# Kernel optimization log

Hardware: AMD Instinct MI355X
Metric: run time of the kernel (lower is better)

Reference implementation:

```python
import jax, jax.numpy as jnp
import numpy as np

EXPERT_NUM = 8
SEQ_LEN = 4096
FREQ_LEN = SEQ_LEN // 2 + 1


def setup_inputs() -> dict:
    key = jax.random.key(0)
    ks = jax.random.split(key, 6)
    B, C = 32, 8
    x = jax.random.normal(ks[0], (B, C, SEQ_LEN), dtype=jnp.float32)
    raw = jax.random.uniform(ks[1], (EXPERT_NUM - 1,), dtype=jnp.float32)
    s1 = 1.0 / np.sqrt(FREQ_LEN)
    W1 = jax.random.uniform(ks[2], (FREQ_LEN, FREQ_LEN), jnp.float32, -s1, s1)
    b1 = jax.random.uniform(ks[3], (FREQ_LEN,), jnp.float32, -s1, s1)
    W2 = jax.random.uniform(ks[4], (EXPERT_NUM, FREQ_LEN), jnp.float32, -s1, s1)
    b2 = jax.random.uniform(ks[5], (EXPERT_NUM,), jnp.float32, -s1, s1)
    return {"x": x, "raw": raw, "W1": W1, "b1": b1, "W2": W2, "b2": b2}


def reference(x, raw, W1, b1, W2, b2):
    # instance norm over seq dim (unbiased variance, like torch.var default)
    x_mean = jnp.mean(x, axis=2, keepdims=True)
    xc = x - x_mean
    n = x.shape[2]
    x_var = jnp.sum(xc * xc, axis=2, keepdims=True) / (n - 1) + 1e-5
    xn = xc / jnp.sqrt(x_var)

    freq_x = jnp.fft.rfft(xn, axis=-1)            # [B, C, F] complex
    F_ = freq_x.shape[-1]

    # sorted sigmoid boundaries -> integer band edges (non-differentiable cast)
    b = jnp.sort(jax.nn.sigmoid(raw))
    boundaries = jnp.concatenate([jnp.zeros(1, x.dtype), b, jnp.ones(1, x.dtype)])
    idx = jnp.floor(jax.lax.stop_gradient(boundaries) * F_).astype(jnp.int32)
    idx = idx.at[-1].set(F_)

    # band-pass masks for all experts at once: [E, F]
    fpos = jnp.arange(F_)
    mask = (fpos[None, :] >= idx[:-1, None]) & (fpos[None, :] < idx[1:, None])

    # per-expert frequency components: [B, E, C, F]
    comp = freq_x[:, None, :, :] * mask[None, :, None, :].astype(freq_x.dtype)
    expert_outputs = jnp.fft.irfft(comp, n=SEQ_LEN, axis=-1)  # [B, E, C, L]

    # gating on channel-averaged magnitude spectrum
    gating_input = jnp.mean(jnp.abs(freq_x), axis=1)          # [B, F]
    h = jax.nn.relu(gating_input @ W1.T + b1)
    gating_scores = jax.nn.softmax(h @ W2.T + b2, axis=-1)    # [B, E]

    # gated combine in frequency domain, then single iFFT
    gate_c = gating_scores.astype(freq_x.dtype)
    combined_freq = jnp.einsum('becf,be->bcf', comp, gate_c)
    combined = jnp.fft.irfft(combined_freq, n=SEQ_LEN, axis=-1)
    combined = combined * jnp.sqrt(x_var) + x_mean
    return combined, boundaries, gating_scores, expert_outputs
```

## Files before the change

kernel.cpp:

```cpp
#include <hip/hip_runtime.h>
#include <hip/hip_bf16.h>


using cplx = float2;
typedef float nfloat2 __attribute__((ext_vector_type(2)));

static constexpr int BB = 32, CCH = 8, LL = 4096, FF = 2049, EE = 8;

static constexpr size_t WS_FREQ  = 0;
static constexpr size_t WS_MEAN  = WS_FREQ + (size_t)BB * CCH * FF * 2;
static constexpr size_t WS_SIGMA = WS_MEAN + 256;
static constexpr size_t WS_H     = WS_SIGMA + 256;
static constexpr size_t WS_IDX   = WS_H + (size_t)BB * FF;
static constexpr size_t WS_EOF   = WS_IDX + 16;

static constexpr size_t OUT_COMB = 0;
static constexpr size_t OUT_BND  = (size_t)BB * CCH * LL;
static constexpr size_t OUT_GATE = OUT_BND + 9;
static constexpr size_t OUT_EXP  = OUT_GATE + (size_t)BB * EE;

__device__ float2 g_W2048[2048];
__device__ float2 g_U[2049];
__device__ int    g_tabcnt = 0;
__device__ float  g_gi[BB * FF];

#define PHI(i) ((i) + ((i) >> 5))
__device__ __forceinline__ int scat(int n) {
  return ((n & 3) << 9) | (((n >> 2) & 7) << 6) | (((n >> 5) & 7) << 3) | (n >> 8);
}

template <bool INV>
__device__ __forceinline__ void dft8(float* zr, float* zi) {
  const float C = 0.70710678118654752f;
  float s0r = zr[0] + zr[4], s0i = zi[0] + zi[4];
  float d0r = zr[0] - zr[4], d0i = zi[0] - zi[4];
  float s1r = zr[2] + zr[6], s1i = zi[2] + zi[6];
  float d1r = zr[2] - zr[6], d1i = zi[2] - zi[6];
  float E0r = s0r + s1r, E0i = s0i + s1i;
  float E2r = s0r - s1r, E2i = s0i - s1i;
  float E1r, E1i, E3r, E3i;
  if (!INV) { E1r = d0r + d1i; E1i = d0i - d1r; E3r = d0r - d1i; E3i = d0i + d1r; }
  else      { E1r = d0r - d1i; E1i = d0i + d1r; E3r = d0r + d1i; E3i = d0i - d1r; }
  float t0r = zr[1] + zr[5], t0i = zi[1] + zi[5];
  float e0r = zr[1] - zr[5], e0i = zi[1] - zi[5];
  float t1r = zr[3] + zr[7], t1i = zi[3] + zi[7];
  float e1r = zr[3] - zr[7], e1i = zi[3] - zi[7];
  float O0r = t0r + t1r, O0i = t0i + t1i;
  float O2r = t0r - t1r, O2i = t0i - t1i;
  float O1r, O1i, O3r, O3i;
  if (!INV) { O1r = e0r + e1i; O1i = e0i - e1r; O3r = e0r - e1i; O3i = e0i + e1r; }
  else      { O1r = e0r - e1i; O1i = e0i + e1r; O3r = e0r + e1i; O3i = e0i - e1r; }
  float w1r, w1i, w2r, w2i, w3r, w3i;
  if (!INV) {
    w1r = C * (O1r + O1i); w1i = C * (O1i - O1r);
    w2r = O2i;             w2i = -O2r;
    w3r = C * (O3i - O3r); w3i = -C * (O3r + O3i);
  } else {
    w1r = C * (O1r - O1i); w1i = C * (O1i + O1r);
    w2r = -O2i;            w2i = O2r;
    w3r = -C * (O3r + O3i); w3i = C * (O3r - O3i);
  }
  zr[0] = E0r + O0r; zi[0] = E0i + O0i;
  zr[4] = E0r - O0r; zi[4] = E0i - O0i;
  zr[1] = E1r + w1r; zi[1] = E1i + w1i;
  zr[5] = E1r - w1r; zi[5] = E1i - w1i;
  zr[2] = E2r + w2r; zi[2] = E2i + w2i;
  zr[6] = E2r - w2r; zi[6] = E2i - w2i;
  zr[3] = E3r + w3r; zi[3] = E3i + w3i;
  zr[7] = E3r - w3r; zi[7] = E3i - w3i;
}

template <bool INV>
__device__ __forceinline__ void dft4(float* zr, float* zi) {
  float s0r = zr[0] + zr[2], s0i = zi[0] + zi[2];
  float d0r = zr[0] - zr[2], d0i = zi[0] - zi[2];
  float s1r = zr[1] + zr[3], s1i = zi[1] + zi[3];
  float d1r = zr[1] - zr[3], d1i = zi[1] - zi[3];
  zr[0] = s0r + s1r; zi[0] = s0i + s1i;
  zr[2] = s0r - s1r; zi[2] = s0i - s1i;
  if (!INV) { zr[1] = d0r + d1i; zi[1] = d0i - d1r; zr[3] = d0r - d1i; zi[3] = d0i + d1r; }
  else      { zr[1] = d0r - d1i; zi[1] = d0i + d1r; zr[3] = d0r + d1i; zi[3] = d0i - d1r; }
}

template <bool INV>
__device__ void fftr8(float* ZR, float* ZI, const cplx* __restrict__ W, int t) {
  float zr[8], zi[8];
  {
    int base = 8 * t;
#pragma unroll
    for (int m = 0; m < 8; ++m) { int i = PHI(base + m); zr[m] = ZR[i]; zi[m] = ZI[i]; }
    dft8<INV>(zr, zi);
#pragma unroll
    for (int m = 0; m < 8; ++m) { int i = PHI(base + m); ZR[i] = zr[m]; ZI[i] = zi[m]; }
  }
  __syncthreads();
  {
    int g = t & 31, p = t >> 5;
    int base = 64 * g + p;
#pragma unroll
    for (int m = 0; m < 8; ++m) { int i = PHI(base + 8 * m); zr[m] = ZR[i]; zi[m] = ZI[i]; }
#pragma unroll
    for (int m = 1; m < 8; ++m) {
      cplx w = W[32 * m * p];
      float wi = INV ? -w.y : w.y;
      float xr = zr[m] * w.x - zi[m] * wi;
      float xi = zr[m] * wi + zi[m] * w.x;
      zr[m] = xr; zi[m] = xi;
    }
    dft8<INV>(zr, zi);
#pragma unroll
    for (int m = 0; m < 8; ++m) { int i = PHI(base + 8 * m); ZR[i] = zr[m]; ZI[i] = zi[m]; }
  }
  __syncthreads();
  {
    int g = t & 3, p = t >> 2;
    int base = 512 * g + p;
#pragma unroll
    for (int m = 0; m < 8; ++m) { int i = PHI(base + 64 * m); zr[m] = ZR[i]; zi[m] = ZI[i]; }
#pragma unroll
    for (int m = 1; m < 8; ++m) {
      cplx w = W[4 * m * p];
      float wi = INV ? -w.y : w.y;
      float xr = zr[m] * w.x - zi[m] * wi;
      float xi = zr[m] * wi + zi[m] * w.x;
      zr[m] = xr; zi[m] = xi;
    }
    dft8<INV>(zr, zi);
#pragma unroll
    for (int m = 0; m < 8; ++m) { int i = PHI(base + 64 * m); ZR[i] = zr[m]; ZI[i] = zi[m]; }
  }
  __syncthreads();
  {
#pragma unroll
    for (int h = 0; h < 2; ++h) {
      int p = t + (h << 8);
      float yr[4], yi[4];
#pragma unroll
      for (int m = 0; m < 4; ++m) { int i = PHI(p + 512 * m); yr[m] = ZR[i]; yi[m] = ZI[i]; }
#pragma unroll
      for (int m = 1; m < 4; ++m) {
        cplx w = W[m * p];
        float wi = INV ? -w.y : w.y;
        float xr = yr[m] * w.x - yi[m] * wi;
        float xi = yr[m] * wi + yi[m] * w.x;
        yr[m] = xr; yi[m] = xi;
      }
      dft4<INV>(yr, yi);
#pragma unroll
      for (int m = 0; m < 4; ++m) { int i = PHI(p + 512 * m); ZR[i] = yr[m]; ZI[i] = yi[m]; }
    }
  }
  __syncthreads();
}

__device__ __forceinline__ void expert_ifft(const float* __restrict__ ws,
                                            float* __restrict__ out,
                                            float* ZR, float* ZI,
                                            int bc, int j, int t) {
  const int b = bc >> 3, c = bc & 7;
  const cplx* freq = (const cplx*)ws + (size_t)bc * FF;
  const int*  idxp = (const int*)(ws + WS_IDX);
  const int lo = idxp[j], hi = idxp[j + 1];

#pragma unroll
  for (int u = 0; u < 8; ++u) {
    int k  = t + (u << 8);
    int km = 2048 - k;
    cplx A = make_float2(0.f, 0.f), Bv = make_float2(0.f, 0.f);
    if (k >= lo && k < hi)   A  = freq[k];
    if (km >= lo && km < hi) Bv = freq[km];
    float Px = A.x - Bv.x, Py = A.y + Bv.y;
    float Qx = A.x + Bv.x, Qy = A.y - Bv.y;
    cplx uk = g_U[k];
    float cs = uk.x, sn = -uk.y;
    float Xox = 0.5f * (cs * Px - sn * Py);
    float Xoy = 0.5f * (cs * Py + sn * Px);
    int i = PHI(scat(k));
    ZR[i] = 0.5f * Qx - Xoy;
    ZI[i] = 0.5f * Qy + Xox;
  }
  __syncthreads();

  fftr8<true>(ZR, ZI, g_W2048, t);

  const float mul = 1.0f / 2048.0f;
  float* op = out + OUT_EXP + (((size_t)(b * EE + j) * CCH + c) * LL);
  if (t == 0) __builtin_nontemporal_store(ZR[PHI(0)] * mul, op);
#pragma unroll
  for (int u = 0; u < 8; ++u) {
    int n = t + (u << 8);
    if (n < 2047) {
      nfloat2 o;
      o.x = ZI[PHI(n)] * mul;
      o.y = ZR[PHI(n + 1)] * mul;
      __builtin_nontemporal_store(o, (nfloat2*)(op + 2 * n + 1));
    } else {
      __builtin_nontemporal_store(ZI[PHI(2047)] * mul, op + 4095);
    }
  }
}

__global__ __launch_bounds__(256) void k_fwd(const float* __restrict__ x,
                                             const float* __restrict__ raw,
                                             float* __restrict__ ws,
                                             float* __restrict__ out) {
  const int p = blockIdx.x, t = threadIdx.x;

  if (p >= 256) {
    if (p < 273) {
      if (__hip_atomic_load(&g_tabcnt, __ATOMIC_RELAXED, __HIP_MEMORY_SCOPE_AGENT) < 17) {
        if (p < 264) {
          int jj = (p - 256) * 256 + t;
          float sn, cs;
          sincosf(-6.283185307179586f * (float)jj / 2048.0f, &sn, &cs);
          g_W2048[jj] = make_float2(cs, sn);
        } else {
          int k = (p - 264) * 256 + t;
          if (k < FF) {
            float sn, cs;
            sincosf(-3.14159265358979323846f * (float)k / 2048.0f, &sn, &cs);
            g_U[k] = make_float2(cs, sn);
          }
        }
        __syncthreads();
        if (t == 0) {
          __threadfence();
          __hip_atomic_fetch_add(&g_tabcnt, 1, __ATOMIC_RELEASE, __HIP_MEMORY_SCOPE_AGENT);
        }
      }
    } else if (p == 273) {
      __shared__ int idx_s[9];
      if (t == 0) {
        float v[7];
        for (int i = 0; i < 7; ++i) v[i] = 1.0f / (1.0f + expf(-raw[i]));
        for (int a = 1; a < 7; ++a) {
          float key = v[a];
          int q = a - 1;
          while (q >= 0 && v[q] > key) { v[q + 1] = v[q]; --q; }
          v[q + 1] = key;
        }
        float bnd[9];
        bnd[0] = 0.0f; bnd[8] = 1.0f;
        for (int i = 0; i < 7; ++i) bnd[i + 1] = v[i];
        int* wi = (int*)(ws + WS_IDX);
        for (int e = 0; e < 9; ++e) {
          int id = (int)floorf(bnd[e] * (float)FF);
          if (e == 8) id = FF;
          idx_s[e] = id;
          wi[e] = id;
          out[OUT_BND + e] = bnd[e];
        }
      }
      __syncthreads();
      int* eof = (int*)(ws + WS_EOF);
      for (int f = t; f < FF; f += 256) {
        int e = 0;
        for (int q = 1; q < 8; ++q)
          if (f >= idx_s[q]) e = q;
        eof[f] = e;
      }
    } else {
      float4* hp = (float4*)(ws + WS_H);
      const float4 z4 = make_float4(0.f, 0.f, 0.f, 0.f);
      for (int i = (p - 274) * 256 + t; i < 16392; i += 8 * 256) hp[i] = z4;
    }
    return;
  }

  __shared__ float ZR[2112], ZI[2112];
  __shared__ float red[8];
  const int bc = p;
  const int b  = bc >> 3;
  const int lane = t & 63, wid = t >> 6;
  const float2* xp2 = (const float2*)(x + (size_t)bc * LL);

  float2 v[8];
  float sum = 0.f;
#pragma unroll
  for (int u = 0; u < 8; ++u) {
    v[u] = xp2[t + (u << 8)];
    sum += v[u].x + v[u].y;
  }
#pragma unroll
  for (int off = 32; off > 0; off >>= 1) sum += __shfl_down(sum, off, 64);
  if (lane == 0) red[wid] = sum;
  __syncthreads();
  const float mean = (red[0] + red[1] + red[2] + red[3]) * (1.0f / 4096.0f);

  float ss = 0.f;
#pragma unroll
  for (int u = 0; u < 8; ++u) {
    float dx = v[u].x - mean, dy = v[u].y - mean;
    ss += dx * dx + dy * dy;
  }
#pragma unroll
  for (int off = 32; off > 0; off >>= 1) ss += __shfl_down(ss, off, 64);
  if (lane == 0) red[4 + wid] = ss;
  __syncthreads();
  const float var   = (red[4] + red[5] + red[6] + red[7]) / 4095.0f + 1e-5f;
  const float sigma = sqrtf(var);
  const float inv   = 1.0f / sigma;
  if (t == 0) {
    ws[WS_MEAN + bc]  = mean;
    ws[WS_SIGMA + bc] = sigma;
  }

#pragma unroll
  for (int u = 0; u < 8; ++u) {
    int n = t + (u << 8);
    int i = PHI(scat(n));
    ZR[i] = (v[u].x - mean) * inv;
    ZI[i] = (v[u].y - mean) * inv;
  }
  if (t == 0) {
    while (__hip_atomic_load(&g_tabcnt, __ATOMIC_ACQUIRE, __HIP_MEMORY_SCOPE_AGENT) < 17) {
      __builtin_amdgcn_s_sleep(8);
    }
  }
  __syncthreads();

  fftr8<false>(ZR, ZI, g_W2048, t);

  cplx* freq = (cplx*)ws + (size_t)bc * FF;
#pragma unroll
  for (int u = 0; u < 9; ++u) {
    int k = t + (u << 8);
    if (k > 2048) break;
    int ka = k & 2047, km = (2048 - k) & 2047;
    float Zkr = ZR[PHI(ka)], Zki = ZI[PHI(ka)];
    float Zmr = ZR[PHI(km)], Zmi = ZI[PHI(km)];
    float fex = 0.5f * (Zkr + Zmr);
    float fey = 0.5f * (Zki - Zmi);
    float fox = 0.5f * (Zki + Zmi);
    float foy = -0.5f * (Zkr - Zmr);
    cplx uk = g_U[k];
    float rx = fex + uk.x * fox - uk.y * foy;
    float ry = fey + uk.x * foy + uk.y * fox;
    freq[k] = make_float2(rx, ry);
    atomicAdd(&g_gi[(size_t)b * FF + k], 0.125f * sqrtf(rx * rx + ry * ry));
  }
}

__global__ __launch_bounds__(256) void k_mid(const float* __restrict__ W1,
                                             float* __restrict__ ws,
                                             float* __restrict__ out) {
  __shared__ float SM[4224];
  const int p = blockIdx.x, t = threadIdx.x;

  if (p < 1089) {
    float* W1s = SM;
    float* gis = SM + 2112;
    const int i0 = (p % 33) * 64;
    const int il = t & 63, bg = t >> 6;
    float acc[8] = {0, 0, 0, 0, 0, 0, 0, 0};
    const int fbeg = (p / 33) * 64;
    const int fend = min(fbeg + 64, FF);
    for (int f0 = fbeg; f0 < fend; f0 += 32) {
      for (int q = t; q < 64 * 32; q += 256) {
        int r = q >> 5, cc = q & 31;
        int gi_i = i0 + r, gf = f0 + cc;
        W1s[r * 33 + cc] = (gi_i < FF && gf < FF) ? W1[(size_t)gi_i * FF + gf] : 0.f;
      }
      for (int q = t; q < 32 * 32; q += 256) {
        int bb = q >> 5, cc = q & 31;
        int gf = f0 + cc;
        gis[bb * 33 + cc] = (gf < FF) ? g_gi[(size_t)bb * FF + gf] : 0.f;
      }
      __syncthreads();
#pragma unroll 8
      for (int cc = 0; cc < 32; ++cc) {
        float wv = W1s[il * 33 + cc];
#pragma unroll
        for (int j = 0; j < 8; ++j) acc[j] += wv * gis[(bg * 8 + j) * 33 + cc];
      }
      __syncthreads();
    }
    int ii = i0 + il;
    if (ii < FF) {
#pragma unroll
      for (int j = 0; j < 8; ++j)
        atomicAdd(&ws[WS_H + (size_t)(bg * 8 + j) * FF + ii], acc[j]);
    }
    return;
  }
  if (p < 1096) return;

  const int e   = p - 1096;
  const int xcd = e & 7, s = e >> 3;
  const int grp = s >> 3, j = s & 7;
  const int bc  = (grp << 3) | xcd;
  expert_ifft(ws, out, SM, SM + 2112, bc, j, t);
}

__global__ __launch_bounds__(256) void k_comb(const float* __restrict__ b1,
                                              const float* __restrict__ W2,
                                              const float* __restrict__ b2,
                                              const float* __restrict__ ws,
                                              float* __restrict__ out) {
  __shared__ float ZR[2112], ZI[2112];
  __shared__ float red[4][8];
  __shared__ float lg[8];
  __shared__ float gates_s[8];
  const int q = blockIdx.x, t = threadIdx.x;
  const int bc = q;
  const int b  = bc >> 3, c = bc & 7;
  const int lane = t & 63, wid = t >> 6;

  {
    int i = q * 256 + t;
    g_gi[i] = 0.f;
    if (i < 32) g_gi[65536 + i] = 0.f;
  }

  float pacc[8] = {0, 0, 0, 0, 0, 0, 0, 0};
  const float* hrow = ws + WS_H + (size_t)b * FF;
  for (int f = t; f < FF; f += 256) {
    float hv = fmaxf(hrow[f] + b1[f], 0.f);
#pragma unroll
    for (int e = 0; e < 8; ++e) pacc[e] += hv * W2[(size_t)e * FF + f];
  }
#pragma unroll
  for (int off = 32; off > 0; off >>= 1) {
#pragma unroll
    for (int e = 0; e < 8; ++e) pacc[e] += __shfl_down(pacc[e], off, 64);
  }
  if (lane == 0) {
#pragma unroll
    for (int e = 0; e < 8; ++e) red[wid][e] = pacc[e];
  }
  __syncthreads();
  if (t < 8) lg[t] = red[0][t] + red[1][t] + red[2][t] + red[3][t] + b2[t];
  __syncthreads();
  if (t < 8) {
    float mx = lg[0];
#pragma unroll
    for (int r2 = 1; r2 < 8; ++r2) mx = fmaxf(mx, lg[r2]);
    float sm = 0.f;
#pragma unroll
    for (int r2 = 0; r2 < 8; ++r2) sm += expf(lg[r2] - mx);
    float g = expf(lg[t] - mx) / sm;
    gates_s[t] = g;
    if (c == 0) out[OUT_GATE + (size_t)b * 8 + t] = g;
  }
  __syncthreads();

  const cplx* freq = (const cplx*)ws + (size_t)bc * FF;
  const int*  eof  = (const int*)(ws + WS_EOF);

#pragma unroll
  for (int u = 0; u < 8; ++u) {
    int k  = t + (u << 8);
    int km = 2048 - k;
    cplx A  = freq[k];
    cplx Bv = freq[km];
    float gk = gates_s[eof[k]], gm = gates_s[eof[km]];
    A.x *= gk; A.y *= gk; Bv.x *= gm; Bv.y *= gm;
    float Px = A.x - Bv.x, Py = A.y + Bv.y;
    float Qx = A.x + Bv.x, Qy = A.y - Bv.y;
    cplx uk = g_U[k];
    float cs = uk.x, sn = -uk.y;
    float Xox = 0.5f * (cs * Px - sn * Py);
    float Xoy = 0.5f * (cs * Py + sn * Px);
    int i = PHI(scat(k));
    ZR[i] = 0.5f * Qx - Xoy;
    ZI[i] = 0.5f * Qy + Xox;
  }
  __syncthreads();

  fftr8<true>(ZR, ZI, g_W2048, t);

  const float mul = ws[WS_SIGMA + bc] * (1.0f / 2048.0f);
  const float add = ws[WS_MEAN + bc];
  nfloat2* op = (nfloat2*)(out + OUT_COMB + (size_t)bc * LL);
#pragma unroll
  for (int u = 0; u < 8; ++u) {
    int n = t + (u << 8);
    nfloat2 o;
    o.x = ZR[PHI(n)] * mul + add;
    o.y = ZI[PHI(n)] * mul + add;
    __builtin_nontemporal_store(o, op + n);
  }
}

extern "C" void kernel_launch(void* const* d_in, const int* in_sizes, int n_in,
                              void* d_out, int out_size, void* d_ws, size_t ws_size,
                              hipStream_t stream) {
  const float* x   = (const float*)d_in[0];
  const float* raw = (const float*)d_in[1];
  const float* W1  = (const float*)d_in[2];
  const float* b1  = (const float*)d_in[3];
  const float* W2  = (const float*)d_in[4];
  const float* b2  = (const float*)d_in[5];
  float* out = (float*)d_out;
  float* ws  = (float*)d_ws;

  k_fwd<<<282, 256, 0, stream>>>(x, raw, ws, out);
  k_mid<<<1096 + 2048, 256, 0, stream>>>(W1, ws, out);
  k_comb<<<256, 256, 0, stream>>>(b1, W2, b2, ws, out);
}
```

Baseline: 130.6 us.

## Fuse ReLU and W2 projection into GEMV blocks, pack two rows per FFT block

The W1 GEMV no longer uses 1089 split-K blocks that atomically accumulate into a zeroed H buffer. It now runs 33 blocks, each covering the full K range for 64 outputs. Each block applies bias and ReLU and computes a partial W2 projection into g_part, which k_comb sums to get the gating logits. This removes the H zeroing, the atomics and the per-row W2 dot products in k_comb. The forward and combine FFT kernels now process two (b,c) rows per 512-thread block, and the expert-iFFT row mapping is adjusted. The risk is that only 33 blocks stream the 16 MB W1 matrix, so GEMV parallelism may be too low to saturate bandwidth.

```diff
diff --git a/kernel.cpp b/kernel.cpp
--- a/kernel.cpp
+++ b/kernel.cpp
@@ -10,8 +10,7 @@
 static constexpr size_t WS_FREQ  = 0;
 static constexpr size_t WS_MEAN  = WS_FREQ + (size_t)BB * CCH * FF * 2;
 static constexpr size_t WS_SIGMA = WS_MEAN + 256;
-static constexpr size_t WS_H     = WS_SIGMA + 256;
-static constexpr size_t WS_IDX   = WS_H + (size_t)BB * FF;
+static constexpr size_t WS_IDX   = WS_SIGMA + 256;
 static constexpr size_t WS_EOF   = WS_IDX + 16;
 
 static constexpr size_t OUT_COMB = 0;
@@ -23,6 +22,7 @@
 __device__ float2 g_U[2049];
 __device__ int    g_tabcnt = 0;
 __device__ float  g_gi[BB * FF];
+__device__ float  g_part[33 * 256];
 
 #define PHI(i) ((i) + ((i) >> 5))
 __device__ __forceinline__ int scat(int n) {
@@ -200,27 +200,32 @@
   }
 }
 
-__global__ __launch_bounds__(256) void k_fwd(const float* __restrict__ x,
+__global__ __launch_bounds__(512) void k_fwd(const float* __restrict__ x,
                                              const float* __restrict__ raw,
                                              float* __restrict__ ws,
                                              float* __restrict__ out) {
   const int p = blockIdx.x, t = threadIdx.x;
 
-  if (p >= 256) {
-    if (p < 273) {
-      if (__hip_atomic_load(&g_tabcnt, __ATOMIC_RELAXED, __HIP_MEMORY_SCOPE_AGENT) < 17) {
-        if (p < 264) {
-          int jj = (p - 256) * 256 + t;
+  if (p >= 128) {
+    if (p < 132) {
+      if (__hip_atomic_load(&g_tabcnt, __ATOMIC_RELAXED, __HIP_MEMORY_SCOPE_AGENT) < 9) {
+        int jj = (p - 128) * 512 + t;
+        float sn, cs;
+        sincosf(-6.283185307179586f * (float)jj / 2048.0f, &sn, &cs);
+        g_W2048[jj] = make_float2(cs, sn);
+        __syncthreads();
+        if (t == 0) {
+          __threadfence();
+          __hip_atomic_fetch_add(&g_tabcnt, 1, __ATOMIC_RELEASE, __HIP_MEMORY_SCOPE_AGENT);
+        }
+      }
+    } else if (p < 137) {
+      if (__hip_atomic_load(&g_tabcnt, __ATOMIC_RELAXED, __HIP_MEMORY_SCOPE_AGENT) < 9) {
+        int k = (p - 132) * 512 + t;
+        if (k < FF) {
           float sn, cs;
-          sincosf(-6.283185307179586f * (float)jj / 2048.0f, &sn, &cs);
-          g_W2048[jj] = make_float2(cs, sn);
-        } else {
-          int k = (p - 264) * 256 + t;
-          if (k < FF) {
-            float sn, cs;
-            sincosf(-3.14159265358979323846f * (float)k / 2048.0f, &sn, &cs);
-            g_U[k] = make_float2(cs, sn);
-          }
+          sincosf(-3.14159265358979323846f * (float)k / 2048.0f, &sn, &cs);
+          g_U[k] = make_float2(cs, sn);
         }
         __syncthreads();
         if (t == 0) {
@@ -228,7 +233,7 @@
           __hip_atomic_fetch_add(&g_tabcnt, 1, __ATOMIC_RELEASE, __HIP_MEMORY_SCOPE_AGENT);
         }
       }
-    } else if (p == 273) {
+    } else {
       __shared__ int idx_s[9];
       if (t == 0) {
         float v[7];
@@ -253,39 +258,37 @@
       }
       __syncthreads();
       int* eof = (int*)(ws + WS_EOF);
-      for (int f = t; f < FF; f += 256) {
+      for (int f = t; f < FF; f += 512) {
         int e = 0;
         for (int q = 1; q < 8; ++q)
           if (f >= idx_s[q]) e = q;
         eof[f] = e;
       }
-    } else {
-      float4* hp = (float4*)(ws + WS_H);
-      const float4 z4 = make_float4(0.f, 0.f, 0.f, 0.f);
-      for (int i = (p - 274) * 256 + t; i < 16392; i += 8 * 256) hp[i] = z4;
     }
     return;
   }
 
-  __shared__ float ZR[2112], ZI[2112];
-  __shared__ float red[8];
-  const int bc = p;
-  const int b  = bc >> 3;
-  const int lane = t & 63, wid = t >> 6;
+  __shared__ float ZR[4224], ZI[4224];
+  __shared__ float red[2][8];
+  const int r   = t >> 8, tl = t & 255;
+  const int bc  = (p << 1) | r;
+  const int b   = bc >> 3;
+  const int roff = r * 2112;
+  const int lane = t & 63, wid = (t >> 6) & 3;
   const float2* xp2 = (const float2*)(x + (size_t)bc * LL);
 
   float2 v[8];
   float sum = 0.f;
 #pragma unroll
   for (int u = 0; u < 8; ++u) {
-    v[u] = xp2[t + (u << 8)];
+    v[u] = xp2[tl + (u << 8)];
     sum += v[u].x + v[u].y;
   }
 #pragma unroll
   for (int off = 32; off > 0; off >>= 1) sum += __shfl_down(sum, off, 64);
-  if (lane == 0) red[wid] = sum;
-  __syncthreads();
-  const float mean = (red[0] + red[1] + red[2] + red[3]) * (1.0f / 4096.0f);
+  if (lane == 0) red[r][wid] = sum;
+  __syncthreads();
+  const float mean = (red[r][0] + red[r][1] + red[r][2] + red[r][3]) * (1.0f / 4096.0f);
 
   float ss = 0.f;
 #pragma unroll
@@ -295,40 +298,40 @@
   }
 #pragma unroll
   for (int off = 32; off > 0; off >>= 1) ss += __shfl_down(ss, off, 64);
-  if (lane == 0) red[4 + wid] = ss;
-  __syncthreads();
-  const float var   = (red[4] + red[5] + red[6] + red[7]) / 4095.0f + 1e-5f;
+  if (lane == 0) red[r][4 + wid] = ss;
+  __syncthreads();
+  const float var   = (red[r][4] + red[r][5] + red[r][6] + red[r][7]) / 4095.0f + 1e-5f;
   const float sigma = sqrtf(var);
   const float inv   = 1.0f / sigma;
-  if (t == 0) {
+  if (tl == 0) {
     ws[WS_MEAN + bc]  = mean;
     ws[WS_SIGMA + bc] = sigma;
   }
 
 #pragma unroll
   for (int u = 0; u < 8; ++u) {
-    int n = t + (u << 8);
-    int i = PHI(scat(n));
+    int n = tl + (u << 8);
+    int i = roff + PHI(scat(n));
     ZR[i] = (v[u].x - mean) * inv;
     ZI[i] = (v[u].y - mean) * inv;
   }
   if (t == 0) {
-    while (__hip_atomic_load(&g_tabcnt, __ATOMIC_ACQUIRE, __HIP_MEMORY_SCOPE_AGENT) < 17) {
+    while (__hip_atomic_load(&g_tabcnt, __ATOMIC_ACQUIRE, __HIP_MEMORY_SCOPE_AGENT) < 9) {
       __builtin_amdgcn_s_sleep(8);
     }
   }
   __syncthreads();
 
-  fftr8<false>(ZR, ZI, g_W2048, t);
+  fftr8<false>(ZR + roff, ZI + roff, g_W2048, tl);
 
   cplx* freq = (cplx*)ws + (size_t)bc * FF;
 #pragma unroll
   for (int u = 0; u < 9; ++u) {
-    int k = t + (u << 8);
+    int k = tl + (u << 8);
     if (k > 2048) break;
     int ka = k & 2047, km = (2048 - k) & 2047;
-    float Zkr = ZR[PHI(ka)], Zki = ZI[PHI(ka)];
-    float Zmr = ZR[PHI(km)], Zmi = ZI[PHI(km)];
+    float Zkr = ZR[roff + PHI(ka)], Zki = ZI[roff + PHI(ka)];
+    float Zmr = ZR[roff + PHI(km)], Zmi = ZI[roff + PHI(km)];
     float fex = 0.5f * (Zkr + Zmr);
     float fey = 0.5f * (Zki - Zmi);
     float fox = 0.5f * (Zki + Zmi);
@@ -342,24 +345,24 @@
 }
 
 __global__ __launch_bounds__(256) void k_mid(const float* __restrict__ W1,
+                                             const float* __restrict__ b1,
+                                             const float* __restrict__ W2,
                                              float* __restrict__ ws,
                                              float* __restrict__ out) {
   __shared__ float SM[4224];
   const int p = blockIdx.x, t = threadIdx.x;
 
-  if (p < 1089) {
+  if (p < 33) {
     float* W1s = SM;
     float* gis = SM + 2112;
-    const int i0 = (p % 33) * 64;
+    const int i0 = p * 64;
     const int il = t & 63, bg = t >> 6;
     float acc[8] = {0, 0, 0, 0, 0, 0, 0, 0};
-    const int fbeg = (p / 33) * 64;
-    const int fend = min(fbeg + 64, FF);
-    for (int f0 = fbeg; f0 < fend; f0 += 32) {
+    for (int f0 = 0; f0 < FF; f0 += 32) {
       for (int q = t; q < 64 * 32; q += 256) {
-        int r = q >> 5, cc = q & 31;
-        int gi_i = i0 + r, gf = f0 + cc;
-        W1s[r * 33 + cc] = (gi_i < FF && gf < FF) ? W1[(size_t)gi_i * FF + gf] : 0.f;
+        int rr = q >> 5, cc = q & 31;
+        int gi_i = i0 + rr, gf = f0 + cc;
+        W1s[rr * 33 + cc] = (gi_i < FF && gf < FF) ? W1[(size_t)gi_i * FF + gf] : 0.f;
       }
       for (int q = t; q < 32 * 32; q += 256) {
         int bb = q >> 5, cc = q & 31;
@@ -375,61 +378,58 @@
       }
       __syncthreads();
     }
-    int ii = i0 + il;
-    if (ii < FF) {
-#pragma unroll
-      for (int j = 0; j < 8; ++j)
-        atomicAdd(&ws[WS_H + (size_t)(bg * 8 + j) * FF + ii], acc[j]);
+    const int ii = i0 + il;
+    float* Hs = SM;
+    const float b1v = (ii < FF) ? b1[ii] : 0.f;
+#pragma unroll
+    for (int j = 0; j < 8; ++j) {
+      float hv = (ii < FF) ? fmaxf(acc[j] + b1v, 0.f) : 0.f;
+      Hs[il * 33 + bg * 8 + j] = hv;
+    }
+    __syncthreads();
+    {
+      const int bq = t >> 3, e = t & 7;
+      const int imax = min(64, FF - i0);
+      float s = 0.f;
+      for (int i2 = 0; i2 < imax; ++i2)
+        s += Hs[i2 * 33 + bq] * W2[(size_t)e * FF + i0 + i2];
+      g_part[p * 256 + t] = s;
     }
     return;
   }
-  if (p < 1096) return;
-
-  const int e   = p - 1096;
+  if (p < 40) return;
+
+  const int e   = p - 40;
   const int xcd = e & 7, s = e >> 3;
-  const int grp = s >> 3, j = s & 7;
-  const int bc  = (grp << 3) | xcd;
+  const int m   = s >> 3, j = s & 7;
+  const int bc  = ((m >> 1) << 4) | (xcd << 1) | (m & 1);
   expert_ifft(ws, out, SM, SM + 2112, bc, j, t);
 }
 
-__global__ __launch_bounds__(256) void k_comb(const float* __restrict__ b1,
-                                              const float* __restrict__ W2,
-                                              const float* __restrict__ b2,
+__global__ __launch_bounds__(512) void k_comb(const float* __restrict__ b2,
                                               const float* __restrict__ ws,
                                               float* __restrict__ out) {
-  __shared__ float ZR[2112], ZI[2112];
-  __shared__ float red[4][8];
+  __shared__ float ZR[4224], ZI[4224];
   __shared__ float lg[8];
   __shared__ float gates_s[8];
   const int q = blockIdx.x, t = threadIdx.x;
-  const int bc = q;
-  const int b  = bc >> 3, c = bc & 7;
-  const int lane = t & 63, wid = t >> 6;
+  const int r = t >> 8, tl = t & 255;
+  const int bc = (q << 1) | r;
+  const int b  = bc >> 3;
+  const int roff = r * 2112;
 
   {
-    int i = q * 256 + t;
+    int i = q * 512 + t;
     g_gi[i] = 0.f;
     if (i < 32) g_gi[65536 + i] = 0.f;
   }
 
-  float pacc[8] = {0, 0, 0, 0, 0, 0, 0, 0};
-  const float* hrow = ws + WS_H + (size_t)b * FF;
-  for (int f = t; f < FF; f += 256) {
-    float hv = fmaxf(hrow[f] + b1[f], 0.f);
-#pragma unroll
-    for (int e = 0; e < 8; ++e) pacc[e] += hv * W2[(size_t)e * FF + f];
-  }
-#pragma unroll
-  for (int off = 32; off > 0; off >>= 1) {
-#pragma unroll
-    for (int e = 0; e < 8; ++e) pacc[e] += __shfl_down(pacc[e], off, 64);
-  }
-  if (lane == 0) {
-#pragma unroll
-    for (int e = 0; e < 8; ++e) red[wid][e] = pacc[e];
-  }
-  __syncthreads();
-  if (t < 8) lg[t] = red[0][t] + red[1][t] + red[2][t] + red[3][t] + b2[t];
+  if (t < 8) {
+    float s = b2[t];
+#pragma unroll
+    for (int p2 = 0; p2 < 33; ++p2) s += g_part[p2 * 256 + b * 8 + t];
+    lg[t] = s;
+  }
   __syncthreads();
   if (t < 8) {
     float mx = lg[0];
@@ -440,7 +440,7 @@
     for (int r2 = 0; r2 < 8; ++r2) sm += expf(lg[r2] - mx);
     float g = expf(lg[t] - mx) / sm;
     gates_s[t] = g;
-    if (c == 0) out[OUT_GATE + (size_t)b * 8 + t] = g;
+    if ((bc & 7) == 0) out[OUT_GATE + (size_t)b * 8 + t] = g;
   }
   __syncthreads();
 
@@ -449,7 +449,7 @@
 
 #pragma unroll
   for (int u = 0; u < 8; ++u) {
-    int k  = t + (u << 8);
+    int k  = tl + (u << 8);
     int km = 2048 - k;
     cplx A  = freq[k];
     cplx Bv = freq[km];
@@ -461,23 +461,23 @@
     float cs = uk.x, sn = -uk.y;
     float Xox = 0.5f * (cs * Px - sn * Py);
     float Xoy = 0.5f * (cs * Py + sn * Px);
-    int i = PHI(scat(k));
+    int i = roff + PHI(scat(k));
     ZR[i] = 0.5f * Qx - Xoy;
     ZI[i] = 0.5f * Qy + Xox;
   }
   __syncthreads();
 
-  fftr8<true>(ZR, ZI, g_W2048, t);
+  fftr8<true>(ZR + roff, ZI + roff, g_W2048, tl);
 
   const float mul = ws[WS_SIGMA + bc] * (1.0f / 2048.0f);
   const float add = ws[WS_MEAN + bc];
   nfloat2* op = (nfloat2*)(out + OUT_COMB + (size_t)bc * LL);
 #pragma unroll
   for (int u = 0; u < 8; ++u) {
-    int n = t + (u << 8);
+    int n = tl + (u << 8);
     nfloat2 o;
-    o.x = ZR[PHI(n)] * mul + add;
-    o.y = ZI[PHI(n)] * mul + add;
+    o.x = ZR[roff + PHI(n)] * mul + add;
+    o.y = ZI[roff + PHI(n)] * mul + add;
     __builtin_nontemporal_store(o, op + n);
   }
 }
@@ -494,7 +494,7 @@
   float* out = (float*)d_out;
   float* ws  = (float*)d_ws;
 
-  k_fwd<<<282, 256, 0, stream>>>(x, raw, ws, out);
-  k_mid<<<1096 + 2048, 256, 0, stream>>>(W1, ws, out);
-  k_comb<<<256, 256, 0, stream>>>(b1, W2, b2, ws, out);
-}
+  k_fwd<<<138, 512, 0, stream>>>(x, raw, ws, out);
+  k_mid<<<40 + 2048, 256, 0, stream>>>(W1, b1, W2, ws, out);
+  k_comb<<<128, 512, 0, stream>>>(b2, ws, out);
+}
```

Measured after the change: 520.1 us. +298.1%, slower.
